# Kernel optimization log

Hardware: AMD Instinct MI355X
Metric: run time of the kernel (lower is better)

## Reference

```python
import jax, jax.numpy as jnp
import numpy as np

N_NODES = 50000
NEG_SLOPE = 0.2  # PyG GATConv default leaky_relu slope


def gat_conv(x, src, dst, W, a_src, a_dst, b, heads, out_ch, concat):
    """PyG-style GATConv. src/dst: [E] edge endpoints (messages flow src->dst)."""
    n = N_NODES
    h = (x @ W).reshape(n, heads, out_ch)            # [N, H, C]
    # per-node attention logits, gathered per edge
    s_src = (h * a_src).sum(-1)                       # [N, H]
    s_dst = (h * a_dst).sum(-1)                       # [N, H]
    e = jax.nn.leaky_relu(s_src[src] + s_dst[dst], NEG_SLOPE)  # [E, H]
    # segment softmax over incoming edges of each dst node
    e_max = jax.ops.segment_max(e, dst, num_segments=n)        # [N, H]
    ex = jnp.exp(e - e_max[dst])                                # [E, H]
    denom = jax.ops.segment_sum(ex, dst, num_segments=n)       # [N, H]
    alpha = ex / denom[dst]                                     # [E, H]
    # scatter-add weighted messages
    out = jax.ops.segment_sum(h[src] * alpha[:, :, None], dst, num_segments=n)  # [N, H, C]
    if concat:
        out = out.reshape(n, heads * out_ch)
    else:
        out = out.mean(axis=1)
    return out + b


def setup_inputs() -> dict:
    key = jax.random.key(0)
    ks = jax.random.split(key, 16)
    n, e = N_NODES, 400000
    in_ch, hidden, out_ch = 3, 64, 32
    x = jax.random.normal(ks[0], (n, in_ch), dtype=jnp.float32)
    edge_index = jax.random.randint(ks[1], (2, e), 0, n, dtype=jnp.int32)

    def glorot(k, shape):
        fan = sum(shape)
        return jax.random.uniform(k, shape, jnp.float32, -1.0, 1.0) * jnp.sqrt(6.0 / fan)

    # layer 1: in=3 -> hidden=64, heads=4, concat
    W1 = glorot(ks[2], (in_ch, 4 * hidden))
    a_src1 = glorot(ks[3], (4, hidden))
    a_dst1 = glorot(ks[4], (4, hidden))
    b1 = jnp.zeros((4 * hidden,), jnp.float32)
    # layer 2: 256 -> 64, heads=4, concat
    W2 = glorot(ks[5], (4 * hidden, 4 * hidden))
    a_src2 = glorot(ks[6], (4, hidden))
    a_dst2 = glorot(ks[7], (4, hidden))
    b2 = jnp.zeros((4 * hidden,), jnp.float32)
    # layer 3: 256 -> 32, heads=1, mean (concat=False)
    W3 = glorot(ks[8], (4 * hidden, out_ch))
    a_src3 = glorot(ks[9], (1, out_ch))
    a_dst3 = glorot(ks[10], (1, out_ch))
    b3 = jnp.zeros((out_ch,), jnp.float32)
    return dict(x=x, edge_index=edge_index,
                W1=W1, a_src1=a_src1, a_dst1=a_dst1, b1=b1,
                W2=W2, a_src2=a_src2, a_dst2=a_dst2, b2=b2,
                W3=W3, a_src3=a_src3, a_dst3=a_dst3, b3=b3)


def reference(x, edge_index,
              W1, a_src1, a_dst1, b1,
              W2, a_src2, a_dst2, b2,
              W3, a_src3, a_dst3, b3):
    n = N_NODES
    loops = jnp.arange(n, dtype=edge_index.dtype)
    src = jnp.concatenate([edge_index[0], loops])  # PyG adds self-loops by default
    dst = jnp.concatenate([edge_index[1], loops])
    h = gat_conv(x, src, dst, W1, a_src1, a_dst1, b1, heads=4, out_ch=64, concat=True)
    h = jax.nn.relu(h)  # dropout is identity in eval mode
    h = gat_conv(h, src, dst, W2, a_src2, a_dst2, b2, heads=4, out_ch=64, concat=True)
    h = jax.nn.relu(h)
    out = gat_conv(h, src, dst, W3, a_src3, a_dst3, b3, heads=1, out_ch=32, concat=False)
    return out
```

## Files before the change

kernel.cpp:

```cpp
#include <hip/hip_runtime.h>
#include <math.h>


#define NEG_SLOPE 0.2f
#define CAP 40

typedef unsigned short u16;
typedef short bf16x8 __attribute__((ext_vector_type(8)));
typedef float floatx4 __attribute__((ext_vector_type(4)));

__device__ __forceinline__ float b2f(u16 u) {
    return __uint_as_float(((unsigned int)u) << 16);
}
__device__ __forceinline__ u16 f2b(float f) {
    unsigned int u = __float_as_uint(f);
    unsigned int r = (u + 0x7fffu + ((u >> 16) & 1u)) >> 16;
    return (u16)r;
}
__device__ __forceinline__ void load16(const u16* g, u16* l) {
    __builtin_amdgcn_global_load_lds(
        (const __attribute__((address_space(1))) void*)g,
        (__attribute__((address_space(3))) void*)l, 16, 0, 0);
}


__device__ __forceinline__ void pack_dev(const float* __restrict__ W,
                                         u16* __restrict__ Bhi,
                                         u16* __restrict__ Blo, int N, int idx) {
    int CT = N / 16;
    int lane = idx & 63;
    int ctkb = idx >> 6;
    int ct = ctkb % CT;
    int kb = ctkb / CT;
    int col = ct * 16 + (lane & 15);
    int k0 = kb * 32 + (lane >> 4) * 8;
#pragma unroll
    for (int j = 0; j < 8; ++j) {
        float w = W[(size_t)(k0 + j) * N + col];
        u16 hi = f2b(w);
        Bhi[(size_t)idx * 8 + j] = hi;
        Blo[(size_t)idx * 8 + j] = f2b(w - b2f(hi));
    }
}


__global__ __launch_bounds__(256) void fill_prep(
    const int* __restrict__ ei,
    const float* __restrict__ W1, const float* __restrict__ as1,
    const float* __restrict__ ad1,
    const float* __restrict__ W2, const float* __restrict__ W3,
    u16* __restrict__ B2h, u16* __restrict__ B2l,
    u16* __restrict__ B3h, u16* __restrict__ B3l,
    float* __restrict__ vsd, int* __restrict__ cursor,
    int* __restrict__ csr, int n, int E) {
    const int tid = threadIdx.x;
    const int tg = blockIdx.x * 256 + tid;
    const int NTH = gridDim.x * 256;
    const int Etot = E + n;
    const int lane = tid & 63;

    if (tg < 8192) {
        pack_dev(W2, B2h, B2l, 256, tg);
    } else if (tg < 9216) {
        pack_dev(W3, B3h, B3l, 32, tg - 8192);
    } else if (tg < 9472) {
        int j = tg - 9216;
        float a_s = as1[j], a_d = ad1[j];
#pragma unroll
        for (int k = 0; k < 3; ++k) {
            float w = W1[k * 256 + j];
            float ps = w * a_s, pd = w * a_d;
#pragma unroll
            for (int o = 32; o > 0; o >>= 1) {
                ps += __shfl_xor(ps, o);
                pd += __shfl_xor(pd, o);
            }
            if (lane == 0) {
                vsd[(j >> 6) * 3 + k] = ps;
                vsd[12 + (j >> 6) * 3 + k] = pd;
            }
        }
    }
    for (int e = tg; e < Etot; e += NTH) {
        int src, dst;
        if (e < E) { src = ei[e]; dst = ei[E + e]; }
        else       { src = e - E; dst = e - E; }
        int old = atomicAdd(&cursor[dst], 1);
        if (old < CAP) csr[dst * CAP + old] = src;
    }
}


__global__ __launch_bounds__(256) void gat_aggregate_l1(const float* __restrict__ x,
                                                        const float* __restrict__ vsd,
                                                        const int* __restrict__ cur,
                                                        const int* __restrict__ csr,
                                                        const float* __restrict__ W1,
                                                        const float* __restrict__ bias,
                                                        u16* __restrict__ outHi, int n) {
    int node = blockIdx.x * 4 + (threadIdx.x >> 6);
    int lane = threadIdx.x & 63;
    if (node >= n) return;
    const int hB = lane & 3;
    const int eL = lane >> 2;
    const int hA = lane >> 4;
    int beg = node * CAP;
    int end = beg + min(cur[node], CAP);

    float vs0 = vsd[hB * 3 + 0], vs1 = vsd[hB * 3 + 1], vs2 = vsd[hB * 3 + 2];
    float vd0 = vsd[12 + hB * 3 + 0], vd1 = vsd[12 + hB * 3 + 1], vd2 = vsd[12 + hB * 3 + 2];
    float xd0 = x[node * 3 + 0], xd1 = x[node * 3 + 1], xd2 = x[node * 3 + 2];
    float sd = fmaf(xd0, vd0, fmaf(xd1, vd1, xd2 * vd2));

    float m = -INFINITY, l = 0.f;
    float ax = 0.f, ay = 0.f, az = 0.f;

    for (int base = beg; base < end; base += 16) {
        int j = base + eL;
        bool valid = (j < end);
        int sj = valid ? csr[j] : 0;
        float x0 = x[sj * 3 + 0];
        float x1 = x[sj * 3 + 1];
        float x2 = x[sj * 3 + 2];
        float logit = -INFINITY;
        if (valid) {
            float xv = fmaf(x0, vs0, fmaf(x1, vs1, x2 * vs2)) + sd;
            logit = (xv > 0.f) ? xv : NEG_SLOPE * xv;
        }
        float cm = logit;
        cm = fmaxf(cm, __shfl_xor(cm, 4));
        cm = fmaxf(cm, __shfl_xor(cm, 8));
        cm = fmaxf(cm, __shfl_xor(cm, 16));
        cm = fmaxf(cm, __shfl_xor(cm, 32));
        float nm = fmaxf(m, cm);
        float scale = __expf(m - nm);
        float ex = valid ? __expf(logit - nm) : 0.f;
        float es = ex;
        es += __shfl_xor(es, 4);
        es += __shfl_xor(es, 8);
        es += __shfl_xor(es, 16);
        es += __shfl_xor(es, 32);
        l = l * scale + es;
        m = nm;
        float sA = __shfl(scale, hA);
        ax *= sA; ay *= sA; az *= sA;

        int cnt = min(16, end - base);
        for (int t = 0; t < cnt; ++t) {
            float a  = __shfl(ex, t * 4 + hA);
            float bx = __shfl(x0, t * 4);
            float by = __shfl(x1, t * 4);
            float bz = __shfl(x2, t * 4);
            ax = fmaf(a, bx, ax);
            ay = fmaf(a, by, ay);
            az = fmaf(a, bz, az);
        }
    }

    float lf = __shfl(l, hA);
    float inv = 1.f / lf;
    ax *= inv; ay *= inv; az *= inv;

    int c = lane * 4;
    const float4 w0 = *(const float4*)&W1[0 * 256 + c];
    const float4 w1 = *(const float4*)&W1[1 * 256 + c];
    const float4 w2 = *(const float4*)&W1[2 * 256 + c];
    const float4 bv = *(const float4*)&bias[c];
    float4 o;
    o.x = fmaxf(fmaf(ax, w0.x, fmaf(ay, w1.x, fmaf(az, w2.x, bv.x))), 0.f);
    o.y = fmaxf(fmaf(ax, w0.y, fmaf(ay, w1.y, fmaf(az, w2.y, bv.y))), 0.f);
    o.z = fmaxf(fmaf(ax, w0.z, fmaf(ay, w1.z, fmaf(az, w2.z, bv.z))), 0.f);
    o.w = fmaxf(fmaf(ax, w0.w, fmaf(ay, w1.w, fmaf(az, w2.w, bv.w))), 0.f);
    ushort4 h4;
    h4.x = f2b(o.x);
    h4.y = f2b(o.y);
    h4.z = f2b(o.z);
    h4.w = f2b(o.w);
    *(ushort4*)&outHi[(size_t)node * 256 + c] = h4;
}


template <int CT, int HEADS>
__global__ __launch_bounds__(512, 4) void gemm_async(const u16* __restrict__ Ahi,
                                                     const u16* __restrict__ Bhi,
                                                     const u16* __restrict__ Blo,
                                                     const float* __restrict__ asrc,
                                                     const float* __restrict__ adst,
                                                     u16* __restrict__ Hb,
                                                     float* __restrict__ ssrc,
                                                     float* __restrict__ sdst, int n) {
    constexpr int THREADS = 512;
    constexpr int BFRAG = CT * 64;
    constexpr int BSZ = BFRAG * 8;
    __shared__ __align__(16) u16 lds[2][2 * BSZ];

    int t = threadIdx.x;
    int w = t >> 6, l = t & 63;
    int m0 = blockIdx.x * 128 + w * 16;
    int lm = l & 15, q = l >> 4;

    int arow = min(m0 + lm, n - 1);
    const u16* aH = Ahi + (size_t)arow * 256 + q * 8;

    floatx4 acc[CT] = {};

    auto stageB = [&](int buf, int kb) {
        u16* L = &lds[buf][0];
        constexpr int BROUNDS = (BFRAG + THREADS - 1) / THREADS;
#pragma unroll
        for (int r = 0; r < BROUNDS; ++r) {
            int u = r * THREADS + t;
            if ((BFRAG % THREADS == 0) || u < BFRAG) {
                size_t off = ((size_t)kb * BFRAG + (size_t)u) * 8;
                u16* Lb = L + (size_t)(r * THREADS + w * 64) * 8;
                load16(Bhi + off, Lb);
                load16(Blo + off, Lb + BSZ);
            }
        }
    };

    stageB(0, 0);
    bf16x8 ahi = *(const bf16x8*)aH;
    __syncthreads();

    for (int kb = 0; kb < 8; ++kb) {
        int cur = kb & 1;
        bf16x8 nhi = ahi;
        if (kb < 7) {
            stageB(cur ^ 1, kb + 1);
            nhi = *(const bf16x8*)(aH + (kb + 1) * 32);
        }
        const u16* L = &lds[cur][0];
#pragma unroll
        for (int ct = 0; ct < CT; ++ct) {
            bf16x8 bhi = *(const bf16x8*)&L[(ct * 64 + l) * 8];
            bf16x8 blo = *(const bf16x8*)&L[BSZ + (ct * 64 + l) * 8];
            acc[ct] = __builtin_amdgcn_mfma_f32_16x16x32_bf16(ahi, bhi, acc[ct], 0, 0, 0);
            acc[ct] = __builtin_amdgcn_mfma_f32_16x16x32_bf16(ahi, blo, acc[ct], 0, 0, 0);
        }
        __syncthreads();
        ahi = nhi;
    }

#pragma unroll
    for (int ct = 0; ct < CT; ++ct) {
#pragma unroll
        for (int r = 0; r < 4; ++r) {
            int row = m0 + q * 4 + r;
            if (row < n)
                Hb[(size_t)row * (CT * 16) + ct * 16 + lm] = f2b(acc[ct][r]);
        }
    }
    constexpr int CPH = CT / HEADS;
    float ps[4][HEADS] = {}, pd[4][HEADS] = {};
#pragma unroll
    for (int h = 0; h < HEADS; ++h) {
#pragma unroll
        for (int j = 0; j < CPH; ++j) {
            int ct = h * CPH + j;
            float a_s = asrc[ct * 16 + lm];
            float a_d = adst[ct * 16 + lm];
#pragma unroll
            for (int r = 0; r < 4; ++r) {
                ps[r][h] = fmaf(acc[ct][r], a_s, ps[r][h]);
                pd[r][h] = fmaf(acc[ct][r], a_d, pd[r][h]);
            }
        }
    }
#pragma unroll
    for (int r = 0; r < 4; ++r)
#pragma unroll
        for (int h = 0; h < HEADS; ++h)
#pragma unroll
            for (int o = 1; o < 16; o <<= 1) {
                ps[r][h] += __shfl_xor(ps[r][h], o);
                pd[r][h] += __shfl_xor(pd[r][h], o);
            }
#pragma unroll
    for (int h = 0; h < HEADS; ++h) {
        if (lm == h) {
#pragma unroll
            for (int r = 0; r < 4; ++r) {
                int row = m0 + q * 4 + r;
                if (row < n) {
                    ssrc[row * HEADS + h] = ps[r][h];
                    sdst[row * HEADS + h] = pd[r][h];
                }
            }
        }
    }
}


__global__ __launch_bounds__(256) void gat_aggregate_m4(const u16* __restrict__ Hb,
                                                        const float* __restrict__ ssrc,
                                                        const float* __restrict__ sdst,
                                                        const int* __restrict__ cur,
                                                        const int* __restrict__ csr,
                                                        const float* __restrict__ bias,
                                                        u16* __restrict__ outHi, int n) {
    int node = blockIdx.x * 4 + (threadIdx.x >> 6);
    int lane = threadIdx.x & 63;
    if (node >= n) return;
    const int hB = lane & 3;
    const int eL = lane >> 2;
    const int hA = lane >> 4;
    int beg = node * CAP;
    int end = beg + min(cur[node], CAP);
    float sd = sdst[node * 4 + hB];
    float m = -INFINITY, l = 0.f;
    float4 acc = make_float4(0.f, 0.f, 0.f, 0.f);

    for (int base = beg; base < end; base += 16) {
        int j = base + eL;
        bool valid = (j < end);
        int sj = valid ? csr[j] : 0;
        float logit = -INFINITY;
        if (valid) {
            float xv = ssrc[sj * 4 + hB] + sd;
            logit = (xv > 0.f) ? xv : NEG_SLOPE * xv;
        }
        float cm = logit;
        cm = fmaxf(cm, __shfl_xor(cm, 4));
        cm = fmaxf(cm, __shfl_xor(cm, 8));
        cm = fmaxf(cm, __shfl_xor(cm, 16));
        cm = fmaxf(cm, __shfl_xor(cm, 32));
        float nm = fmaxf(m, cm);
        float scale = __expf(m - nm);
        float ex = valid ? __expf(logit - nm) : 0.f;
        float es = ex;
        es += __shfl_xor(es, 4);
        es += __shfl_xor(es, 8);
        es += __shfl_xor(es, 16);
        es += __shfl_xor(es, 32);
        l = l * scale + es;
        m = nm;
        float sA = __shfl(scale, hA);
        acc.x *= sA; acc.y *= sA; acc.z *= sA; acc.w *= sA;

        int cnt = min(16, end - base);
        for (int t = 0; t < cnt; t += 4) {
#pragma unroll
            for (int u = 0; u < 4; ++u) {
                int tt = t + u;
                float a = __shfl(ex, tt * 4 + hA);
                int s = __shfl(sj, tt * 4);
                ushort4 hv = *(const ushort4*)&Hb[(size_t)s * 256 + lane * 4];
                acc.x = fmaf(a, b2f(hv.x), acc.x);
                acc.y = fmaf(a, b2f(hv.y), acc.y);
                acc.z = fmaf(a, b2f(hv.z), acc.z);
                acc.w = fmaf(a, b2f(hv.w), acc.w);
            }
        }
    }
    float lf = __shfl(l, hA);
    float inv = 1.f / lf;
    const float4 bv = *(const float4*)&bias[lane * 4];
    float4 o;
    o.x = fmaxf(fmaf(acc.x, inv, bv.x), 0.f);
    o.y = fmaxf(fmaf(acc.y, inv, bv.y), 0.f);
    o.z = fmaxf(fmaf(acc.z, inv, bv.z), 0.f);
    o.w = fmaxf(fmaf(acc.w, inv, bv.w), 0.f);
    ushort4 h4;
    h4.x = f2b(o.x);
    h4.y = f2b(o.y);
    h4.z = f2b(o.z);
    h4.w = f2b(o.w);
    *(ushort4*)&outHi[(size_t)node * 256 + lane * 4] = h4;
}


__global__ __launch_bounds__(256) void gat_aggregate_h1(const u16* __restrict__ Hb,
                                                        const float* __restrict__ ssrc,
                                                        const float* __restrict__ sdst,
                                                        const int* __restrict__ cur,
                                                        const int* __restrict__ csr,
                                                        const float* __restrict__ bias,
                                                        float* __restrict__ out, int n) {
    int node = blockIdx.x * 4 + (threadIdx.x >> 6);
    int lane = threadIdx.x & 63;
    if (node >= n) return;
    int dg = min(cur[node], CAP);
    int beg = node * CAP;
    float sd = sdst[node];

    bool valid = (lane < dg);
    int sj = valid ? csr[beg + lane] : 0;
    float logit = -INFINITY;
    if (valid) {
        float xv = ssrc[sj] + sd;
        logit = (xv > 0.f) ? xv : NEG_SLOPE * xv;
    }
    float cm = logit;
#pragma unroll
    for (int o = 32; o > 0; o >>= 1) cm = fmaxf(cm, __shfl_xor(cm, o));
    float ex = valid ? __expf(logit - cm) : 0.f;
    float l = ex;
#pragma unroll
    for (int o = 32; o > 0; o >>= 1) l += __shfl_xor(l, o);

    const int eh = lane >> 5;
    const int ch = lane & 31;
    float acc = 0.f;
    for (int t = 0; t < dg; t += 8) {
#pragma unroll
        for (int u = 0; u < 4; ++u) {
            int e = t + u * 2 + eh;
            float a = __shfl(ex, e & 63);
            int s = __shfl(sj, e & 63);
            if (e < dg) acc = fmaf(a, b2f(Hb[(size_t)s * 32 + ch]), acc);
        }
    }
    acc += __shfl_xor(acc, 32);
    if (lane < 32) out[(size_t)node * 32 + lane] = acc / l + bias[lane];
}


extern "C" void kernel_launch(void* const* d_in, const int* in_sizes, int n_in,
                              void* d_out, int out_size, void* d_ws, size_t ws_size,
                              hipStream_t stream) {
    const float* x   = (const float*)d_in[0];
    const int*   ei  = (const int*)d_in[1];
    const float* W1  = (const float*)d_in[2];
    const float* as1 = (const float*)d_in[3];
    const float* ad1 = (const float*)d_in[4];
    const float* b1  = (const float*)d_in[5];
    const float* W2  = (const float*)d_in[6];
    const float* as2 = (const float*)d_in[7];
    const float* ad2 = (const float*)d_in[8];
    const float* b2  = (const float*)d_in[9];
    const float* W3  = (const float*)d_in[10];
    const float* as3 = (const float*)d_in[11];
    const float* ad3 = (const float*)d_in[12];
    const float* b3  = (const float*)d_in[13];
    float* out = (float*)d_out;

    const int n = in_sizes[0] / 3;
    const int E = in_sizes[1] / 2;
    const int Etot = E + n;

    char* ws = (char*)d_ws;
    u16* Fhi  = (u16*)ws;    ws += (size_t)n * 256 * sizeof(u16);
    u16* Hb   = (u16*)ws;    ws += (size_t)n * 256 * sizeof(u16);
    u16* Hb3  = (u16*)ws;    ws += (size_t)n * 32 * sizeof(u16);
    u16* B2h  = (u16*)ws;    ws += (size_t)8 * 16 * 64 * 8 * sizeof(u16);
    u16* B2l  = (u16*)ws;    ws += (size_t)8 * 16 * 64 * 8 * sizeof(u16);
    u16* B3h  = (u16*)ws;    ws += (size_t)8 * 2 * 64 * 8 * sizeof(u16);
    u16* B3l  = (u16*)ws;    ws += (size_t)8 * 2 * 64 * 8 * sizeof(u16);
    float* ssrc = (float*)ws;  ws += (size_t)n * 4 * sizeof(float);
    float* sdst = (float*)ws;  ws += (size_t)n * 4 * sizeof(float);
    float* vsd  = (float*)ws;  ws += 32 * sizeof(float);
    int* cursor = (int*)ws;    ws += (size_t)n * sizeof(int);
    int* csr    = (int*)ws;    ws += (size_t)n * CAP * sizeof(int);

    hipMemsetAsync(cursor, 0, (size_t)n * sizeof(int), stream);

    int eblocks = (Etot + 255) / 256;
    int nb4 = (n + 3) / 4;
    int nb128 = (n + 127) / 128;

    fill_prep<<<eblocks, 256, 0, stream>>>(ei, W1, as1, ad1, W2, W3,
                                           B2h, B2l, B3h, B3l, vsd,
                                           cursor, csr, n, E);

    gat_aggregate_l1<<<nb4, 256, 0, stream>>>(x, vsd, cursor, csr, W1, b1,
                                              Fhi, n);

    gemm_async<16, 4><<<nb128, 512, 0, stream>>>(Fhi, B2h, B2l, as2, ad2,
                                                 Hb, ssrc, sdst, n);

    gat_aggregate_m4<<<nb4, 256, 0, stream>>>(Hb, ssrc, sdst, cursor, csr,
                                              b2, Fhi, n);

    gemm_async<2, 1><<<nb128, 512, 0, stream>>>(Fhi, B3h, B3l, as3, ad3,
                                                Hb3, ssrc, sdst, n);

    gat_aggregate_h1<<<nb4, 256, 0, stream>>>(Hb3, ssrc, sdst, cursor, csr,
                                              b3, out, n);
}
```

Baseline: 233.6 us.

## Fuse layer-2 aggregation with layer-3 projection GEMM in one kernel

Merges the layer-2 attention aggregation kernel with the following small layer-3 GEMM (256->32) and its attention-logit computation. Each wave aggregates 16 nodes in sequence, shuffles the bf16 results into MFMA A-fragments in registers, and multiplies them against B3 staged in LDS. This avoids writing the 256-wide layer-2 output to global memory and reading it back, and drops one kernel launch. In exchange each wave processes 16 nodes serially, so there are fewer waves in flight to hide gather latency, and new ssrc3/sdst3 buffers are added.

```diff
diff --git a/kernel.cpp b/kernel.cpp
--- a/kernel.cpp
+++ b/kernel.cpp
@@ -6,6 +6,7 @@
 #define CAP 40
 
 typedef unsigned short u16;
+typedef unsigned int u32;
 typedef short bf16x8 __attribute__((ext_vector_type(8)));
 typedef float floatx4 __attribute__((ext_vector_type(4)));
 
@@ -292,81 +293,163 @@
 }
 
 
-__global__ __launch_bounds__(256) void gat_aggregate_m4(const u16* __restrict__ Hb,
-                                                        const float* __restrict__ ssrc,
-                                                        const float* __restrict__ sdst,
-                                                        const int* __restrict__ cur,
-                                                        const int* __restrict__ csr,
-                                                        const float* __restrict__ bias,
-                                                        u16* __restrict__ outHi, int n) {
-    int node = blockIdx.x * 4 + (threadIdx.x >> 6);
-    int lane = threadIdx.x & 63;
-    if (node >= n) return;
+__global__ __launch_bounds__(256, 4) void agg_m4_g3(
+    const u16* __restrict__ Hb,
+    const float* __restrict__ ssrc, const float* __restrict__ sdst,
+    const int* __restrict__ cur, const int* __restrict__ csr,
+    const float* __restrict__ bias2,
+    const u16* __restrict__ B3h, const u16* __restrict__ B3l,
+    const float* __restrict__ as3, const float* __restrict__ ad3,
+    u16* __restrict__ Hb3, float* __restrict__ ssrc3,
+    float* __restrict__ sdst3, int n) {
+    constexpr int BSZ3 = 8 * 2 * 64 * 8;
+    __shared__ __align__(16) u16 sB[2 * BSZ3];
+
+    const int t = threadIdx.x;
+    const int w = t >> 6;
+    const int lane = t & 63;
+    const int m0 = blockIdx.x * 64 + w * 16;
+    const int lm = lane & 15, q = lane >> 4;
+
+#pragma unroll
+    for (int r = 0; r < 4; ++r) {
+        int u = r * 256 + t;
+        u16* Ldst = sB + (size_t)(r * 256 + w * 64) * 8;
+        load16(B3h + (size_t)u * 8, Ldst);
+        load16(B3l + (size_t)u * 8, Ldst + BSZ3);
+    }
+
     const int hB = lane & 3;
     const int eL = lane >> 2;
     const int hA = lane >> 4;
-    int beg = node * CAP;
-    int end = beg + min(cur[node], CAP);
-    float sd = sdst[node * 4 + hB];
-    float m = -INFINITY, l = 0.f;
-    float4 acc = make_float4(0.f, 0.f, 0.f, 0.f);
-
-    for (int base = beg; base < end; base += 16) {
-        int j = base + eL;
-        bool valid = (j < end);
-        int sj = valid ? csr[j] : 0;
-        float logit = -INFINITY;
-        if (valid) {
-            float xv = ssrc[sj * 4 + hB] + sd;
-            logit = (xv > 0.f) ? xv : NEG_SLOPE * xv;
-        }
-        float cm = logit;
-        cm = fmaxf(cm, __shfl_xor(cm, 4));
-        cm = fmaxf(cm, __shfl_xor(cm, 8));
-        cm = fmaxf(cm, __shfl_xor(cm, 16));
-        cm = fmaxf(cm, __shfl_xor(cm, 32));
-        float nm = fmaxf(m, cm);
-        float scale = __expf(m - nm);
-        float ex = valid ? __expf(logit - nm) : 0.f;
-        float es = ex;
-        es += __shfl_xor(es, 4);
-        es += __shfl_xor(es, 8);
-        es += __shfl_xor(es, 16);
-        es += __shfl_xor(es, 32);
-        l = l * scale + es;
-        m = nm;
-        float sA = __shfl(scale, hA);
-        acc.x *= sA; acc.y *= sA; acc.z *= sA; acc.w *= sA;
-
-        int cnt = min(16, end - base);
-        for (int t = 0; t < cnt; t += 4) {
-#pragma unroll
-            for (int u = 0; u < 4; ++u) {
-                int tt = t + u;
-                float a = __shfl(ex, tt * 4 + hA);
-                int s = __shfl(sj, tt * 4);
-                ushort4 hv = *(const ushort4*)&Hb[(size_t)s * 256 + lane * 4];
-                acc.x = fmaf(a, b2f(hv.x), acc.x);
-                acc.y = fmaf(a, b2f(hv.y), acc.y);
-                acc.z = fmaf(a, b2f(hv.z), acc.z);
-                acc.w = fmaf(a, b2f(hv.w), acc.w);
-            }
-        }
-    }
-    float lf = __shfl(l, hA);
-    float inv = 1.f / lf;
-    const float4 bv = *(const float4*)&bias[lane * 4];
-    float4 o;
-    o.x = fmaxf(fmaf(acc.x, inv, bv.x), 0.f);
-    o.y = fmaxf(fmaf(acc.y, inv, bv.y), 0.f);
-    o.z = fmaxf(fmaf(acc.z, inv, bv.z), 0.f);
-    o.w = fmaxf(fmaf(acc.w, inv, bv.w), 0.f);
-    ushort4 h4;
-    h4.x = f2b(o.x);
-    h4.y = f2b(o.y);
-    h4.z = f2b(o.z);
-    h4.w = f2b(o.w);
-    *(ushort4*)&outHi[(size_t)node * 256 + lane * 4] = h4;
+    const float4 bv = *(const float4*)&bias2[lane * 4];
+
+    bf16x8 abuf[8];
+    for (int i = 0; i < 16; ++i) {
+        int node = m0 + i;
+        float4 o = make_float4(0.f, 0.f, 0.f, 0.f);
+        if (node < n) {
+            int beg = node * CAP;
+            int end = beg + min(cur[node], CAP);
+            float sd = sdst[node * 4 + hB];
+            float m = -INFINITY, l = 0.f;
+            float4 acc4 = make_float4(0.f, 0.f, 0.f, 0.f);
+
+            for (int base = beg; base < end; base += 16) {
+                int j = base + eL;
+                bool valid = (j < end);
+                int sj = valid ? csr[j] : 0;
+                float logit = -INFINITY;
+                if (valid) {
+                    float xv = ssrc[sj * 4 + hB] + sd;
+                    logit = (xv > 0.f) ? xv : NEG_SLOPE * xv;
+                }
+                float cm = logit;
+                cm = fmaxf(cm, __shfl_xor(cm, 4));
+                cm = fmaxf(cm, __shfl_xor(cm, 8));
+                cm = fmaxf(cm, __shfl_xor(cm, 16));
+                cm = fmaxf(cm, __shfl_xor(cm, 32));
+                float nm = fmaxf(m, cm);
+                float scale = __expf(m - nm);
+                float ex = valid ? __expf(logit - nm) : 0.f;
+                float es = ex;
+                es += __shfl_xor(es, 4);
+                es += __shfl_xor(es, 8);
+                es += __shfl_xor(es, 16);
+                es += __shfl_xor(es, 32);
+                l = l * scale + es;
+                m = nm;
+                float sA = __shfl(scale, hA);
+                acc4.x *= sA; acc4.y *= sA; acc4.z *= sA; acc4.w *= sA;
+
+                int cnt = min(16, end - base);
+                for (int tt = 0; tt < cnt; tt += 4) {
+#pragma unroll
+                    for (int u = 0; u < 4; ++u) {
+                        int e = tt + u;
+                        float a = __shfl(ex, e * 4 + hA);
+                        int s = __shfl(sj, e * 4);
+                        ushort4 hv = *(const ushort4*)&Hb[(size_t)s * 256 + lane * 4];
+                        acc4.x = fmaf(a, b2f(hv.x), acc4.x);
+                        acc4.y = fmaf(a, b2f(hv.y), acc4.y);
+                        acc4.z = fmaf(a, b2f(hv.z), acc4.z);
+                        acc4.w = fmaf(a, b2f(hv.w), acc4.w);
+                    }
+                }
+            }
+            float lf = __shfl(l, hA);
+            float inv = 1.f / lf;
+            o.x = fmaxf(fmaf(acc4.x, inv, bv.x), 0.f);
+            o.y = fmaxf(fmaf(acc4.y, inv, bv.y), 0.f);
+            o.z = fmaxf(fmaf(acc4.z, inv, bv.z), 0.f);
+            o.w = fmaxf(fmaf(acc4.w, inv, bv.w), 0.f);
+        }
+        u32 p0 = ((u32)f2b(o.y) << 16) | f2b(o.x);
+        u32 p1 = ((u32)f2b(o.w) << 16) | f2b(o.z);
+#pragma unroll
+        for (int kb = 0; kb < 8; ++kb) {
+            int s0 = kb * 8 + q * 2;
+            u32 a0 = __shfl(p0, s0);
+            u32 a1 = __shfl(p1, s0);
+            u32 a2 = __shfl(p0, s0 + 1);
+            u32 a3 = __shfl(p1, s0 + 1);
+            if (lm == i) {
+                union { uint4 u4; bf16x8 v; } cv;
+                cv.u4 = make_uint4(a0, a1, a2, a3);
+                abuf[kb] = cv.v;
+            }
+        }
+    }
+
+    __syncthreads();
+
+    floatx4 acc[2] = {};
+#pragma unroll
+    for (int kb = 0; kb < 8; ++kb) {
+#pragma unroll
+        for (int ct = 0; ct < 2; ++ct) {
+            const u16* base = sB + (size_t)((kb * 2 + ct) * 64 + lane) * 8;
+            bf16x8 bhi = *(const bf16x8*)base;
+            bf16x8 blo = *(const bf16x8*)(base + BSZ3);
+            acc[ct] = __builtin_amdgcn_mfma_f32_16x16x32_bf16(abuf[kb], bhi, acc[ct], 0, 0, 0);
+            acc[ct] = __builtin_amdgcn_mfma_f32_16x16x32_bf16(abuf[kb], blo, acc[ct], 0, 0, 0);
+        }
+    }
+
+#pragma unroll
+    for (int ct = 0; ct < 2; ++ct) {
+#pragma unroll
+        for (int r = 0; r < 4; ++r) {
+            int row = m0 + q * 4 + r;
+            if (row < n)
+                Hb3[(size_t)row * 32 + ct * 16 + lm] = f2b(acc[ct][r]);
+        }
+    }
+    float ps[4] = {}, pd[4] = {};
+#pragma unroll
+    for (int ct = 0; ct < 2; ++ct) {
+        float a_s = as3[ct * 16 + lm];
+        float a_d = ad3[ct * 16 + lm];
+#pragma unroll
+        for (int r = 0; r < 4; ++r) {
+            ps[r] = fmaf(acc[ct][r], a_s, ps[r]);
+            pd[r] = fmaf(acc[ct][r], a_d, pd[r]);
+        }
+    }
+#pragma unroll
+    for (int r = 0; r < 4; ++r)
+#pragma unroll
+        for (int o = 1; o < 16; o <<= 1) {
+            ps[r] += __shfl_xor(ps[r], o);
+            pd[r] += __shfl_xor(pd[r], o);
+        }
+    if (lm == 0) {
+#pragma unroll
+        for (int r = 0; r < 4; ++r) {
+            int row = m0 + q * 4 + r;
+            if (row < n) { ssrc3[row] = ps[r]; sdst3[row] = pd[r]; }
+        }
+    }
 }
 
 
@@ -449,6 +532,8 @@
     u16* B3l  = (u16*)ws;    ws += (size_t)8 * 2 * 64 * 8 * sizeof(u16);
     float* ssrc = (float*)ws;  ws += (size_t)n * 4 * sizeof(float);
     float* sdst = (float*)ws;  ws += (size_t)n * 4 * sizeof(float);
+    float* ssrc3 = (float*)ws; ws += (size_t)n * sizeof(float);
+    float* sdst3 = (float*)ws; ws += (size_t)n * sizeof(float);
     float* vsd  = (float*)ws;  ws += 32 * sizeof(float);
     int* cursor = (int*)ws;    ws += (size_t)n * sizeof(int);
     int* csr    = (int*)ws;    ws += (size_t)n * CAP * sizeof(int);
@@ -457,6 +542,7 @@
 
     int eblocks = (Etot + 255) / 256;
     int nb4 = (n + 3) / 4;
+    int nb64 = (n + 63) / 64;
     int nb128 = (n + 127) / 128;
 
     fill_prep<<<eblocks, 256, 0, stream>>>(ei, W1, as1, ad1, W2, W3,
@@ -469,12 +555,10 @@
     gemm_async<16, 4><<<nb128, 512, 0, stream>>>(Fhi, B2h, B2l, as2, ad2,
                                                  Hb, ssrc, sdst, n);
 
-    gat_aggregate_m4<<<nb4, 256, 0, stream>>>(Hb, ssrc, sdst, cursor, csr,
-                                              b2, Fhi, n);
-
-    gemm_async<2, 1><<<nb128, 512, 0, stream>>>(Fhi, B3h, B3l, as3, ad3,
-                                                Hb3, ssrc, sdst, n);
-
-    gat_aggregate_h1<<<nb4, 256, 0, stream>>>(Hb3, ssrc, sdst, cursor, csr,
+    agg_m4_g3<<<nb64, 256, 0, stream>>>(Hb, ssrc, sdst, cursor, csr, b2,
+                                        B3h, B3l, as3, ad3,
+                                        Hb3, ssrc3, sdst3, n);
+
+    gat_aggregate_h1<<<nb4, 256, 0, stream>>>(Hb3, ssrc3, sdst3, cursor, csr,
                                               b3, out, n);
 }
```

New measurement: 249.2 us. 1.07x slower.
